# Kernel tuning notes

Measured on AMD Instinct MI355X. Metric: run time of the kernel, lower is better.

## Reference

```python
import jax, jax.numpy as jnp
import numpy as np

NUM_LAYERS = 2
SEQ_LEN = 128
HIDDEN = 512
OUTPUT = 512
BATCH = 512


def setup_inputs() -> dict:
    key = jax.random.key(0)
    ks = jax.random.split(key, 12)
    k = 1.0 / np.sqrt(HIDDEN)
    u = lambda kk, shape: jax.random.uniform(kk, shape, jnp.float32, -k, k)
    return {
        "x": jax.random.normal(ks[0], (BATCH, HIDDEN), jnp.float32),
        # stacked per-layer LSTM params, PyTorch gate order (i, f, g, o)
        "W_ih": u(ks[1], (NUM_LAYERS, 4 * HIDDEN, HIDDEN)),
        "W_hh": u(ks[2], (NUM_LAYERS, 4 * HIDDEN, HIDDEN)),
        "b_ih": u(ks[3], (NUM_LAYERS, 4 * HIDDEN)),
        "b_hh": u(ks[4], (NUM_LAYERS, 4 * HIDDEN)),
        # 3-layer MLP head
        "fc1_w": u(ks[5], (HIDDEN, HIDDEN)),
        "fc1_b": u(ks[6], (HIDDEN,)),
        "fc2_w": u(ks[7], (HIDDEN, HIDDEN)),
        "fc2_b": u(ks[8], (HIDDEN,)),
        "fc3_w": u(ks[9], (OUTPUT, HIDDEN)),
        "fc3_b": u(ks[10], (OUTPUT,)),
    }


def reference(x, W_ih, W_hh, b_ih, b_hh, fc1_w, fc1_b, fc2_w, fc2_b, fc3_w, fc3_b):
    B, H = x.shape
    L = W_ih.shape[0]
    h0 = jnp.zeros((L, B, H), x.dtype)
    c0 = jnp.zeros((L, B, H), x.dtype)

    def step(carry, _):
        h, c, inp = carry  # h,c: [L,B,H]; inp: [B,H]
        x_l = inp
        hs, cs = [], []
        for l in range(L):  # small fixed layer loop
            gates = x_l @ W_ih[l].T + b_ih[l] + h[l] @ W_hh[l].T + b_hh[l]
            i, f, g, o = jnp.split(gates, 4, axis=-1)
            c_new = jax.nn.sigmoid(f) * c[l] + jax.nn.sigmoid(i) * jnp.tanh(g)
            h_new = jax.nn.sigmoid(o) * jnp.tanh(c_new)
            hs.append(h_new)
            cs.append(c_new)
            x_l = h_new
        h = jnp.stack(hs)
        c = jnp.stack(cs)
        h_sum = h.sum(0)  # torch.sum(h_t, 0) over layers
        return (h, c, h_sum), h_sum  # next input is summed hidden

    _, outs = jax.lax.scan(step, (h0, c0, x), None, length=SEQ_LEN)
    out = jnp.transpose(outs, (1, 0, 2))  # [B, seq_len, H]
    out = jax.nn.relu(out @ fc1_w.T + fc1_b)
    out = jax.nn.relu(out @ fc2_w.T + fc2_b)
    out = out @ fc3_w.T + fc3_b  # [B, seq_len, output_size]
    return out
```

## Files before the change

### kernel.cpp

```cpp
#include <hip/hip_runtime.h>
#include <cstdint>
#include <cstddef>


using u16 = unsigned short;
typedef __attribute__((ext_vector_type(8))) _Float16 f16x8;
typedef __attribute__((ext_vector_type(4))) float f32x4;

__device__ __forceinline__ u16 f2h(float f) {
    union { _Float16 h; u16 u; } v; v.h = (_Float16)f; return v.u;
}
__device__ __forceinline__ float h2f(u16 u) {
    union { u16 u; _Float16 h; } v; v.u = u; return (float)v.h;
}
__device__ __forceinline__ float tanh_fast(float v) {
    float a = fabsf(v);
    float t = __expf(-2.f * a);
    float r = (1.f - t) / (1.f + t);
    return copysignf(r, v);
}
__device__ __forceinline__ float sigmoid_fast(float v) {
    return 1.f / (1.f + __expf(-v));
}

__device__ __forceinline__ void gl_lds16(const u16* g, char* l) {
    __builtin_amdgcn_global_load_lds((const __attribute__((address_space(1))) char*)(const char*)g,
                                     (__attribute__((address_space(3))) char*)l, 16, 0, 0);
}

__device__ __forceinline__ f16x8 lds_read_sw(const u16* tile, int row, int cu) {
    int unit = (row << 3) | (cu ^ (row & 7));
    return *(const f16x8*)&tile[unit << 3];
}

__global__ __launch_bounds__(256) void prepack(
    const float* __restrict__ W_ih, const float* __restrict__ W_hh,
    const float* __restrict__ b_ih, const float* __restrict__ b_hh,
    const float* __restrict__ fc1w, const float* __restrict__ fc2w, const float* __restrict__ fc3w,
    u16* __restrict__ Bpack, float* __restrict__ bsumv, u16* __restrict__ fcw)
{
    int stride = gridDim.x * blockDim.x;
    int tid0 = blockIdx.x * blockDim.x + threadIdx.x;
    for (int idx = tid0; idx < 2 * 2048 * 1024; idx += stride) {
        int l = idx >> 21;
        int rem = idx & ((1 << 21) - 1);
        int np = rem >> 10;
        int k = rem & 1023;
        int n = (np & 3) * 512 + (np >> 2);
        float v = (k < 512) ? W_ih[((size_t)l * 2048 + n) * 512 + k]
                            : W_hh[((size_t)l * 2048 + n) * 512 + (k - 512)];
        Bpack[idx] = f2h(v);
    }
    for (int idx = tid0; idx < 2 * 2048; idx += stride) {
        int l = idx >> 11;
        int np = idx & 2047;
        int n = (np & 3) * 512 + (np >> 2);
        bsumv[idx] = b_ih[l * 2048 + n] + b_hh[l * 2048 + n];
    }
    for (int idx = tid0; idx < 3 * 512 * 512; idx += stride) {
        const float* w = idx < 262144 ? fc1w : (idx < 524288 ? fc2w : fc3w);
        fcw[idx] = f2h(w[idx & 262143]);
    }
}

__global__ __launch_bounds__(256) void initbufs(
    const float* __restrict__ x, u16* __restrict__ A0_0, u16* __restrict__ A1_0,
    float* __restrict__ c0, float* __restrict__ c1, float* __restrict__ gb0)
{
    int stride = gridDim.x * blockDim.x;
    int tid0 = blockIdx.x * blockDim.x + threadIdx.x;
    for (int idx = tid0; idx < 512 * 512; idx += stride) {
        int row = idx >> 9, col = idx & 511;
        size_t b = (size_t)row * 1024;
        A0_0[b + col] = f2h(x[idx]);
        A1_0[b + 512 + col] = 0;
        c0[idx] = 0.f;
        c1[idx] = 0.f;
    }
    for (int idx = tid0; idx < 1048576; idx += stride) gb0[idx] = 0.f;
}

template <int IS_L1>
__global__ __launch_bounds__(256) void lstm_phase(
    const u16* __restrict__ Ax, const u16* __restrict__ Ah, int hoffH,
    const u16* __restrict__ Wc, const u16* __restrict__ Wp,
    const float* __restrict__ gbufR, float* __restrict__ gbufW,
    const float* __restrict__ bsumv, float* __restrict__ cbuf,
    u16* __restrict__ hdst, const u16* __restrict__ h0src,
    u16* __restrict__ hsumdst, u16* __restrict__ seqdst)
{
    __shared__ char smem[49152];

    const int id = blockIdx.x;
    const bool isPartial = id >= 256;
    const int rid = id & 255;
    const int xcd = rid & 7, slot = rid >> 3;
    const int nb = xcd * 4 + (slot & 3);
    const int rg = slot >> 2;
    const int n0 = nb * 64;
    const int row0 = rg * 64;
    const int tile = rg * 32 + nb;

    const u16* Abase = isPartial ? Ah : Ax;
    const int xoff = isPartial ? hoffH : 0;
    const u16* Wbase = isPartial ? Wp : Wc;

    const int tid = threadIdx.x;
    const int lane = tid & 63, wid = tid >> 6;
    const int wm = (wid >> 1) * 32, wn = (wid & 1) * 32;
    const int fm = lane & 15, q = lane >> 4;

    const int s0 = wid * 128 + lane, s1 = s0 + 64;
    const int r0s = s0 >> 3, c0s = ((s0 & 7) ^ (r0s & 7)) << 3;
    const int r1s = s1 >> 3, c1s = ((s1 & 7) ^ (r1s & 7)) << 3;
    const size_t aO0 = (size_t)(row0 + r0s) * 1024 + xoff + c0s;
    const size_t aO1 = (size_t)(row0 + r1s) * 1024 + xoff + c1s;
    const size_t bO0 = (size_t)(n0 + r0s) * 1024 + c0s;
    const size_t bO1 = (size_t)(n0 + r1s) * 1024 + c1s;
    const int d0 = wid * 2048, d1 = d0 + 1024;

    f32x4 acc[2][2];
    acc[0][0] = (f32x4)0.f; acc[0][1] = (f32x4)0.f;
    acc[1][0] = (f32x4)0.f; acc[1][1] = (f32x4)0.f;

    auto stage = [&](char* buf, int k0) {
        gl_lds16(Abase + aO0 + k0, buf + d0);
        gl_lds16(Abase + aO1 + k0, buf + d1);
        gl_lds16(Wbase + bO0 + k0, buf + 8192 + d0);
        gl_lds16(Wbase + bO1 + k0, buf + 8192 + d1);
    };

    char* p0 = smem;
    char* p1 = smem + 16384;
    char* p2 = smem + 32768;

    stage(p0, 0);
    stage(p1, 64);

    for (int c = 0; c < 8; ++c) {
        if (c < 7) asm volatile("s_waitcnt vmcnt(4)" ::: "memory");
        else       asm volatile("s_waitcnt vmcnt(0)" ::: "memory");
        __builtin_amdgcn_s_barrier();
        if (c < 6) stage(p2, (c + 2) * 64);
        __builtin_amdgcn_sched_barrier(0);

        const u16* sA = (const u16*)p0;
        const u16* sB = (const u16*)(p0 + 8192);

#pragma unroll
        for (int kf = 0; kf < 2; ++kf) {
            const int cu = kf * 4 + q;
            f16x8 b0 = lds_read_sw(sB, wn + fm, cu);
            f16x8 b1 = lds_read_sw(sB, wn + 16 + fm, cu);
            f16x8 a0 = lds_read_sw(sA, wm + fm, cu);
            f16x8 a1 = lds_read_sw(sA, wm + 16 + fm, cu);
            acc[0][0] = __builtin_amdgcn_mfma_f32_16x16x32_f16(a0, b0, acc[0][0], 0, 0, 0);
            acc[0][1] = __builtin_amdgcn_mfma_f32_16x16x32_f16(a0, b1, acc[0][1], 0, 0, 0);
            acc[1][0] = __builtin_amdgcn_mfma_f32_16x16x32_f16(a1, b0, acc[1][0], 0, 0, 0);
            acc[1][1] = __builtin_amdgcn_mfma_f32_16x16x32_f16(a1, b1, acc[1][1], 0, 0, 0);
        }

        char* t = p0; p0 = p1; p1 = p2; p2 = t;
    }

    if (isPartial) {
        float* dst = gbufW + (size_t)tile * 4096 + wid * 1024 + lane * 4;
        *(f32x4*)(dst +   0) = acc[0][0];
        *(f32x4*)(dst + 256) = acc[0][1];
        *(f32x4*)(dst + 512) = acc[1][0];
        *(f32x4*)(dst + 768) = acc[1][1];
        return;
    }

    {
        const float* src = gbufR + (size_t)tile * 4096 + wid * 1024 + lane * 4;
        acc[0][0] += *(const f32x4*)(src +   0);
        acc[0][1] += *(const f32x4*)(src + 256);
        acc[1][0] += *(const f32x4*)(src + 512);
        acc[1][1] += *(const f32x4*)(src + 768);
    }

    __syncthreads();
    float* sG = (float*)smem;
#pragma unroll
    for (int m = 0; m < 2; ++m)
#pragma unroll
        for (int n = 0; n < 2; ++n)
#pragma unroll
            for (int r = 0; r < 4; ++r) {
                int row = wm + m * 16 + q * 4 + r;
                int col = wn + n * 16 + fm;
                sG[row * 68 + col] = acc[m][n][r];
            }
    __syncthreads();

#pragma unroll
    for (int j = 0; j < 4; ++j) {
        int cell = tid + j * 256;
        int row = cell >> 4, hc = cell & 15;
        const float4 g4 = *(const float4*)&sG[row * 68 + hc * 4];
        const float4 b4 = *(const float4*)&bsumv[n0 + hc * 4];
        float gi = g4.x + b4.x, gf = g4.y + b4.y, gg = g4.z + b4.z, go = g4.w + b4.w;
        int grow = row0 + row;
        int ghc = (n0 >> 2) + hc;
        int cidx = grow * 512 + ghc;
        float c_old = cbuf[cidx];
        float is = sigmoid_fast(gi);
        float fs = sigmoid_fast(gf);
        float os = sigmoid_fast(go);
        float gt = tanh_fast(gg);
        float cn = fs * c_old + is * gt;
        float hn = os * tanh_fast(cn);
        cbuf[cidx] = cn;
        u16 hh = f2h(hn);
        size_t ab = (size_t)grow * 1024;
        if (!IS_L1) {
            hdst[ab + ghc] = hh;
        } else {
            hdst[ab + 512 + ghc] = hh;
            float h0v = h2f(h0src[ab + ghc]);
            float hs = h0v + hn;
            hsumdst[ab + ghc] = f2h(hs);
            seqdst[(size_t)grow * 512 + ghc] = f2h(hs);
        }
    }
}

template <int RELU, int FINAL>
__global__ __launch_bounds__(256) void mlp_gemm(
    const u16* __restrict__ A, const u16* __restrict__ Bw, const float* __restrict__ bias,
    u16* __restrict__ yh, float* __restrict__ yf32)
{
    __shared__ char smem[36864];
    u16* sA = (u16*)smem;
    u16* sB = (u16*)(smem + 9216);

    const int tid = threadIdx.x;
    const int lane = tid & 63, wid = tid >> 6;
    const int row0 = blockIdx.y * 64;
    const int n0 = blockIdx.x * 128;
    const int wn = wid * 32;
    const int fm = lane & 15;
    const int fkbase = (lane >> 4) * 8;

    f32x4 acc[4][2];
#pragma unroll
    for (int m = 0; m < 4; ++m) { acc[m][0] = (f32x4)0.f; acc[m][1] = (f32x4)0.f; }

    for (int kk = 0; kk < 8; ++kk) {
        const int k0 = kk * 64;
        __syncthreads();
#pragma unroll
        for (int r = 0; r < 2; ++r) {
            int c = tid + r * 256;
            int row = c >> 3, cc = (c & 7) * 8;
            *(f16x8*)&sA[row * 72 + cc] = *(const f16x8*)&A[(size_t)(row0 + row) * 512 + k0 + cc];
        }
#pragma unroll
        for (int r = 0; r < 4; ++r) {
            int c = tid + r * 256;
            int row = c >> 3, cc = (c & 7) * 8;
            *(f16x8*)&sB[row * 72 + cc] = *(const f16x8*)&Bw[(size_t)(n0 + row) * 512 + k0 + cc];
        }
        __syncthreads();
#pragma unroll
        for (int kf = 0; kf < 2; ++kf) {
            const int kb = kf * 32 + fkbase;
            f16x8 b0 = *(const f16x8*)&sB[(wn + fm) * 72 + kb];
            f16x8 b1 = *(const f16x8*)&sB[(wn + 16 + fm) * 72 + kb];
#pragma unroll
            for (int m = 0; m < 4; ++m) {
                f16x8 ah = *(const f16x8*)&sA[(m * 16 + fm) * 72 + kb];
                acc[m][0] = __builtin_amdgcn_mfma_f32_16x16x32_f16(ah, b0, acc[m][0], 0, 0, 0);
                acc[m][1] = __builtin_amdgcn_mfma_f32_16x16x32_f16(ah, b1, acc[m][1], 0, 0, 0);
            }
        }
    }

    __syncthreads();
    float* sG = (float*)smem;
#pragma unroll
    for (int m = 0; m < 4; ++m)
#pragma unroll
        for (int n = 0; n < 2; ++n)
#pragma unroll
            for (int r = 0; r < 4; ++r) {
                int row = m * 16 + (lane >> 4) * 4 + r;
                int col = wn + n * 16 + fm;
                sG[row * 132 + col] = acc[m][n][r];
            }
    __syncthreads();

    const int row = tid >> 2;
    const int cg = (tid & 3) * 32;
    const size_t r = (size_t)row0 + row;
#pragma unroll
    for (int c = cg; c < cg + 32; c += 4) {
        float4 g = *(const float4*)&sG[row * 132 + c];
        float4 b = *(const float4*)&bias[n0 + c];
        float v0 = g.x + b.x, v1 = g.y + b.y, v2 = g.z + b.z, v3 = g.w + b.w;
        if (RELU) {
            v0 = fmaxf(v0, 0.f); v1 = fmaxf(v1, 0.f); v2 = fmaxf(v2, 0.f); v3 = fmaxf(v3, 0.f);
        }
        if (!FINAL) {
            ushort4 p;
            p.x = f2h(v0); p.y = f2h(v1); p.z = f2h(v2); p.w = f2h(v3);
            *(ushort4*)&yh[r * 512 + n0 + c] = p;
        } else {
            int tt = (int)(r >> 9), bb = (int)(r & 511);
            float4 o; o.x = v0; o.y = v1; o.z = v2; o.w = v3;
            *(float4*)&yf32[((size_t)bb * 128 + tt) * 512 + n0 + c] = o;
        }
    }
}

extern "C" void kernel_launch(void* const* d_in, const int* in_sizes, int n_in,
                              void* d_out, int out_size, void* d_ws, size_t ws_size,
                              hipStream_t stream) {
    const float* x    = (const float*)d_in[0];
    const float* W_ih = (const float*)d_in[1];
    const float* W_hh = (const float*)d_in[2];
    const float* b_ih = (const float*)d_in[3];
    const float* b_hh = (const float*)d_in[4];
    const float* fc1w = (const float*)d_in[5];
    const float* fc1b = (const float*)d_in[6];
    const float* fc2w = (const float*)d_in[7];
    const float* fc2b = (const float*)d_in[8];
    const float* fc3w = (const float*)d_in[9];
    const float* fc3b = (const float*)d_in[10];

    char* ws = (char*)d_ws;
    u16* Bpack = (u16*)(ws);
    u16* fcw   = (u16*)(ws + 8388608);
    float* bsum = (float*)(ws + 9961472);
    u16* A0[2] = { (u16*)(ws + 9977856),  (u16*)(ws + 11026432) };
    u16* A1[2] = { (u16*)(ws + 12075008), (u16*)(ws + 13123584) };
    float* c0 = (float*)(ws + 14172160);
    float* c1 = (float*)(ws + 15220736);
    u16* seqb = (u16*)(ws + 20463616);
    float* gb[2] = { (float*)(ws + 87572480), (float*)(ws + 87572480 + 4194304) };
    u16* y1   = (u16*)(ws + 87572480);
    float* out = (float*)d_out;

    prepack<<<dim3(512), dim3(256), 0, stream>>>(W_ih, W_hh, b_ih, b_hh, fc1w, fc2w, fc3w,
                                                 Bpack, bsum, fcw);
    initbufs<<<dim3(512), dim3(256), 0, stream>>>(x, A0[0], A1[0], c0, c1, gb[0]);

    const int LSTR = 2048 * 1024;
    for (int s = 0; s < 256; ++s) {
        int t = s >> 1, layer = s & 1, cur = t & 1, nxt = cur ^ 1;
        float* gR = gb[s & 1];
        float* gW = gb[(s + 1) & 1];
        if (!layer) {
            lstm_phase<0><<<dim3(512), dim3(256), 0, stream>>>(
                A0[cur], A1[cur], 512, Bpack, Bpack + LSTR + 512,
                gR, gW, bsum, c0,
                A1[cur], nullptr, nullptr, nullptr);
        } else {
            lstm_phase<1><<<dim3(512), dim3(256), 0, stream>>>(
                A1[cur], A1[cur], 0, Bpack + LSTR, Bpack + 512,
                gR, gW, bsum + 2048, c1,
                A1[nxt], A1[cur], A0[nxt], seqb + (size_t)t * 262144);
        }
    }

    mlp_gemm<1, 0><<<dim3(4, 1024), dim3(256), 0, stream>>>(seqb, fcw, fc1b, y1, nullptr);
    mlp_gemm<1, 0><<<dim3(4, 1024), dim3(256), 0, stream>>>(y1, fcw + 512 * 512, fc2b, seqb, nullptr);
    mlp_gemm<0, 1><<<dim3(4, 1024), dim3(256), 0, stream>>>(seqb, fcw + 2 * 512 * 512, fc3b, nullptr, out);
}
```

Measured before the change: 2.023 ms.

## Load LSTM weight fragments directly to registers and fuse gate epilogue via shuffles

The weight operand is no longer staged through LDS. Each lane now loads its MFMA B fragments straight from global memory into double-buffered registers, which halves the LDS footprint and the per-chunk LDS traffic. The epilogue replaces the shared-memory transpose and its two barriers with lane shuffles that gather the i,f,g,o gates into each lane. s_setprio is wrapped around the MFMA block. The trade-off is that global weight loads are now uncoalesced 16-byte per-lane reads, and the vmcnt counts must match the new outstanding load totals.

```diff
diff --git a/kernel.cpp b/kernel.cpp
--- a/kernel.cpp
+++ b/kernel.cpp
@@ -89,7 +89,7 @@
     u16* __restrict__ hdst, const u16* __restrict__ h0src,
     u16* __restrict__ hsumdst, u16* __restrict__ seqdst)
 {
-    __shared__ char smem[49152];
+    __shared__ char smem[24576];
 
     const int id = blockIdx.x;
     const bool isPartial = id >= 256;
@@ -115,9 +115,10 @@
     const int r1s = s1 >> 3, c1s = ((s1 & 7) ^ (r1s & 7)) << 3;
     const size_t aO0 = (size_t)(row0 + r0s) * 1024 + xoff + c0s;
     const size_t aO1 = (size_t)(row0 + r1s) * 1024 + xoff + c1s;
-    const size_t bO0 = (size_t)(n0 + r0s) * 1024 + c0s;
-    const size_t bO1 = (size_t)(n0 + r1s) * 1024 + c1s;
     const int d0 = wid * 2048, d1 = d0 + 1024;
+
+    const u16* pwA = Wbase + (size_t)(n0 + wn + fm) * 1024 + q * 8;
+    const u16* pwB = pwA + 16 * 1024;
 
     f32x4 acc[2][2];
     acc[0][0] = (f32x4)0.f; acc[0][1] = (f32x4)0.f;
@@ -126,41 +127,53 @@
     auto stage = [&](char* buf, int k0) {
         gl_lds16(Abase + aO0 + k0, buf + d0);
         gl_lds16(Abase + aO1 + k0, buf + d1);
-        gl_lds16(Wbase + bO0 + k0, buf + 8192 + d0);
-        gl_lds16(Wbase + bO1 + k0, buf + 8192 + d1);
     };
 
-    char* p0 = smem;
-    char* p1 = smem + 16384;
-    char* p2 = smem + 32768;
-
-    stage(p0, 0);
-    stage(p1, 64);
-
+    char* bufp[3] = { smem, smem + 8192, smem + 16384 };
+
+    f16x8 w00[2], w01[2], w10[2], w11[2];
+
+    stage(bufp[0], 0);
+    stage(bufp[1], 64);
+    w00[0] = *(const f16x8*)(pwA + 0);
+    w10[0] = *(const f16x8*)(pwA + 32);
+    w01[0] = *(const f16x8*)(pwB + 0);
+    w11[0] = *(const f16x8*)(pwB + 32);
+
+#pragma unroll
     for (int c = 0; c < 8; ++c) {
-        if (c < 7) asm volatile("s_waitcnt vmcnt(4)" ::: "memory");
-        else       asm volatile("s_waitcnt vmcnt(0)" ::: "memory");
+        if (c < 7) asm volatile("s_waitcnt vmcnt(6)" ::: "memory");
+        else       asm volatile("s_waitcnt vmcnt(4)" ::: "memory");
         __builtin_amdgcn_s_barrier();
-        if (c < 6) stage(p2, (c + 2) * 64);
+        if (c + 2 < 8) stage(bufp[(c + 2) % 3], (c + 2) * 64);
+        if (c + 1 < 8) {
+            const int k = (c + 1) * 64;
+            const int p = (c + 1) & 1;
+            w00[p] = *(const f16x8*)(pwA + k);
+            w10[p] = *(const f16x8*)(pwA + k + 32);
+            w01[p] = *(const f16x8*)(pwB + k);
+            w11[p] = *(const f16x8*)(pwB + k + 32);
+        }
         __builtin_amdgcn_sched_barrier(0);
 
-        const u16* sA = (const u16*)p0;
-        const u16* sB = (const u16*)(p0 + 8192);
-
-#pragma unroll
-        for (int kf = 0; kf < 2; ++kf) {
-            const int cu = kf * 4 + q;
-            f16x8 b0 = lds_read_sw(sB, wn + fm, cu);
-            f16x8 b1 = lds_read_sw(sB, wn + 16 + fm, cu);
-            f16x8 a0 = lds_read_sw(sA, wm + fm, cu);
-            f16x8 a1 = lds_read_sw(sA, wm + 16 + fm, cu);
-            acc[0][0] = __builtin_amdgcn_mfma_f32_16x16x32_f16(a0, b0, acc[0][0], 0, 0, 0);
-            acc[0][1] = __builtin_amdgcn_mfma_f32_16x16x32_f16(a0, b1, acc[0][1], 0, 0, 0);
-            acc[1][0] = __builtin_amdgcn_mfma_f32_16x16x32_f16(a1, b0, acc[1][0], 0, 0, 0);
-            acc[1][1] = __builtin_amdgcn_mfma_f32_16x16x32_f16(a1, b1, acc[1][1], 0, 0, 0);
-        }
-
-        char* t = p0; p0 = p1; p1 = p2; p2 = t;
+        const u16* sA = (const u16*)bufp[c % 3];
+        const int p = c & 1;
+
+        f16x8 a00 = lds_read_sw(sA, wm + fm, q);
+        f16x8 a10 = lds_read_sw(sA, wm + 16 + fm, q);
+        f16x8 a01 = lds_read_sw(sA, wm + fm, 4 + q);
+        f16x8 a11 = lds_read_sw(sA, wm + 16 + fm, 4 + q);
+
+        __builtin_amdgcn_s_setprio(1);
+        acc[0][0] = __builtin_amdgcn_mfma_f32_16x16x32_f16(a00, w00[p], acc[0][0], 0, 0, 0);
+        acc[0][1] = __builtin_amdgcn_mfma_f32_16x16x32_f16(a00, w01[p], acc[0][1], 0, 0, 0);
+        acc[1][0] = __builtin_amdgcn_mfma_f32_16x16x32_f16(a10, w00[p], acc[1][0], 0, 0, 0);
+        acc[1][1] = __builtin_amdgcn_mfma_f32_16x16x32_f16(a10, w01[p], acc[1][1], 0, 0, 0);
+        acc[0][0] = __builtin_amdgcn_mfma_f32_16x16x32_f16(a01, w10[p], acc[0][0], 0, 0, 0);
+        acc[0][1] = __builtin_amdgcn_mfma_f32_16x16x32_f16(a01, w11[p], acc[0][1], 0, 0, 0);
+        acc[1][0] = __builtin_amdgcn_mfma_f32_16x16x32_f16(a11, w10[p], acc[1][0], 0, 0, 0);
+        acc[1][1] = __builtin_amdgcn_mfma_f32_16x16x32_f16(a11, w11[p], acc[1][1], 0, 0, 0);
+        __builtin_amdgcn_s_setprio(0);
     }
 
     if (isPartial) {
@@ -180,30 +193,34 @@
         acc[1][1] += *(const f32x4*)(src + 768);
     }
 
-    __syncthreads();
-    float* sG = (float*)smem;
+    const int j = fm & 3;
+    const int hcl = fm >> 2;
 #pragma unroll
     for (int m = 0; m < 2; ++m)
 #pragma unroll
-        for (int n = 0; n < 2; ++n)
-#pragma unroll
-            for (int r = 0; r < 4; ++r) {
-                int row = wm + m * 16 + q * 4 + r;
-                int col = wn + n * 16 + fm;
-                sG[row * 68 + col] = acc[m][n][r];
-            }
-    __syncthreads();
-
-#pragma unroll
-    for (int j = 0; j < 4; ++j) {
-        int cell = tid + j * 256;
-        int row = cell >> 4, hc = cell & 15;
-        const float4 g4 = *(const float4*)&sG[row * 68 + hc * 4];
-        const float4 b4 = *(const float4*)&bsumv[n0 + hc * 4];
-        float gi = g4.x + b4.x, gf = g4.y + b4.y, gg = g4.z + b4.z, go = g4.w + b4.w;
-        int grow = row0 + row;
-        int ghc = (n0 >> 2) + hc;
-        int cidx = grow * 512 + ghc;
+    for (int n = 0; n < 2; ++n) {
+        float v0 = acc[m][n][0], v1 = acc[m][n][1], v2 = acc[m][n][2], v3 = acc[m][n][3];
+        float t0 = __shfl_xor(v1, 1), t1 = __shfl_xor(v0, 1);
+        float t2 = __shfl_xor(v3, 1), t3 = __shfl_xor(v2, 1);
+        bool b1 = (j & 1) != 0;
+        float u0 = b1 ? t0 : v0;
+        float u1 = b1 ? v1 : t1;
+        float u2 = b1 ? t2 : v2;
+        float u3 = b1 ? v3 : t3;
+        t0 = __shfl_xor(u2, 2); t1 = __shfl_xor(u3, 2);
+        t2 = __shfl_xor(u0, 2); t3 = __shfl_xor(u1, 2);
+        bool b2 = (j & 2) != 0;
+        float g0 = b2 ? t0 : u0;
+        float g1 = b2 ? t1 : u1;
+        float g2 = b2 ? u2 : t2;
+        float g3 = b2 ? u3 : t3;
+
+        const int row = row0 + wm + m * 16 + q * 4 + j;
+        const int ghc = ((n0 + wn) >> 2) + n * 4 + hcl;
+        const float4 b4 = *(const float4*)&bsumv[n0 + wn + n * 16 + hcl * 4];
+        float gi = g0 + b4.x, gf = g1 + b4.y, gg = g2 + b4.z, go = g3 + b4.w;
+
+        const int cidx = row * 512 + ghc;
         float c_old = cbuf[cidx];
         float is = sigmoid_fast(gi);
         float fs = sigmoid_fast(gf);
@@ -213,7 +230,7 @@
         float hn = os * tanh_fast(cn);
         cbuf[cidx] = cn;
         u16 hh = f2h(hn);
-        size_t ab = (size_t)grow * 1024;
+        const size_t ab = (size_t)row * 1024;
         if (!IS_L1) {
             hdst[ab + ghc] = hh;
         } else {
@@ -221,7 +238,7 @@
             float h0v = h2f(h0src[ab + ghc]);
             float hs = h0v + hn;
             hsumdst[ab + ghc] = f2h(hs);
-            seqdst[(size_t)grow * 512 + ghc] = f2h(hs);
+            seqdst[(size_t)row * 512 + ghc] = f2h(hs);
         }
     }
 }
```

New measurement: 3.392 ms. +67.7%, slower.

## Double-buffer MLP GEMM tiles with direct global-to-LDS loads and XOR swizzle

Applied to the files above, without the earlier changes.

Rewrites the MLP GEMM main loop so the next K-tile loads directly from global memory into a second LDS buffer while the MFMA work runs on the current one. The padded LDS layout is replaced by an XOR-swizzled layout to avoid bank conflicts. This removes one barrier per iteration and the register round-trip for tile loads. In exchange it doubles the LDS footprint, which may reduce occupancy.

```diff
diff --git a/kernel.cpp b/kernel.cpp
--- a/kernel.cpp
+++ b/kernel.cpp
@@ -231,53 +231,74 @@
     const u16* __restrict__ A, const u16* __restrict__ Bw, const float* __restrict__ bias,
     u16* __restrict__ yh, float* __restrict__ yf32)
 {
-    __shared__ char smem[36864];
-    u16* sA = (u16*)smem;
-    u16* sB = (u16*)(smem + 9216);
+    __shared__ char smem[49152];
 
     const int tid = threadIdx.x;
     const int lane = tid & 63, wid = tid >> 6;
     const int row0 = blockIdx.y * 64;
     const int n0 = blockIdx.x * 128;
     const int wn = wid * 32;
-    const int fm = lane & 15;
-    const int fkbase = (lane >> 4) * 8;
+    const int fm = lane & 15, q = lane >> 4;
+
+    const int sA0 = wid * 128 + lane, sA1 = sA0 + 64;
+    const int rA0 = sA0 >> 3, cA0 = ((sA0 & 7) ^ (rA0 & 7)) << 3;
+    const int rA1 = sA1 >> 3, cA1 = ((sA1 & 7) ^ (rA1 & 7)) << 3;
+    const size_t aO0 = (size_t)(row0 + rA0) * 512 + cA0;
+    const size_t aO1 = (size_t)(row0 + rA1) * 512 + cA1;
+    const int sB0 = wid * 256 + lane;
+    int rB[4], cB[4];
+#pragma unroll
+    for (int i = 0; i < 4; ++i) {
+        int s = sB0 + i * 64;
+        rB[i] = s >> 3; cB[i] = ((s & 7) ^ (rB[i] & 7)) << 3;
+    }
+    const size_t bO0 = (size_t)(n0 + rB[0]) * 512 + cB[0];
+    const size_t bO1 = (size_t)(n0 + rB[1]) * 512 + cB[1];
+    const size_t bO2 = (size_t)(n0 + rB[2]) * 512 + cB[2];
+    const size_t bO3 = (size_t)(n0 + rB[3]) * 512 + cB[3];
+    const int dA0 = wid * 2048, dA1 = dA0 + 1024;
+    const int dB0 = 8192 + wid * 4096;
 
     f32x4 acc[4][2];
 #pragma unroll
     for (int m = 0; m < 4; ++m) { acc[m][0] = (f32x4)0.f; acc[m][1] = (f32x4)0.f; }
 
-    for (int kk = 0; kk < 8; ++kk) {
-        const int k0 = kk * 64;
-        __syncthreads();
-#pragma unroll
-        for (int r = 0; r < 2; ++r) {
-            int c = tid + r * 256;
-            int row = c >> 3, cc = (c & 7) * 8;
-            *(f16x8*)&sA[row * 72 + cc] = *(const f16x8*)&A[(size_t)(row0 + row) * 512 + k0 + cc];
-        }
-#pragma unroll
-        for (int r = 0; r < 4; ++r) {
-            int c = tid + r * 256;
-            int row = c >> 3, cc = (c & 7) * 8;
-            *(f16x8*)&sB[row * 72 + cc] = *(const f16x8*)&Bw[(size_t)(n0 + row) * 512 + k0 + cc];
-        }
-        __syncthreads();
+    auto stage = [&](char* buf, int k0) {
+        gl_lds16(A + aO0 + k0, buf + dA0);
+        gl_lds16(A + aO1 + k0, buf + dA1);
+        gl_lds16(Bw + bO0 + k0, buf + dB0);
+        gl_lds16(Bw + bO1 + k0, buf + dB0 + 1024);
+        gl_lds16(Bw + bO2 + k0, buf + dB0 + 2048);
+        gl_lds16(Bw + bO3 + k0, buf + dB0 + 3072);
+    };
+
+    char* bufs[2] = { smem, smem + 24576 };
+
+    stage(bufs[0], 0);
+    __syncthreads();
+
+    for (int c = 0; c < 8; ++c) {
+        if (c + 1 < 8) stage(bufs[(c + 1) & 1], (c + 1) * 64);
+
+        const u16* sA = (const u16*)bufs[c & 1];
+        const u16* sB = (const u16*)(bufs[c & 1] + 8192);
+
 #pragma unroll
         for (int kf = 0; kf < 2; ++kf) {
-            const int kb = kf * 32 + fkbase;
-            f16x8 b0 = *(const f16x8*)&sB[(wn + fm) * 72 + kb];
-            f16x8 b1 = *(const f16x8*)&sB[(wn + 16 + fm) * 72 + kb];
+            const int cu = kf * 4 + q;
+            f16x8 b0 = lds_read_sw(sB, wn + fm, cu);
+            f16x8 b1 = lds_read_sw(sB, wn + 16 + fm, cu);
 #pragma unroll
             for (int m = 0; m < 4; ++m) {
-                f16x8 ah = *(const f16x8*)&sA[(m * 16 + fm) * 72 + kb];
+                f16x8 ah = lds_read_sw(sA, m * 16 + fm, cu);
                 acc[m][0] = __builtin_amdgcn_mfma_f32_16x16x32_f16(ah, b0, acc[m][0], 0, 0, 0);
                 acc[m][1] = __builtin_amdgcn_mfma_f32_16x16x32_f16(ah, b1, acc[m][1], 0, 0, 0);
             }
         }
-    }
-
-    __syncthreads();
+
+        __syncthreads();
+    }
+
     float* sG = (float*)smem;
 #pragma unroll
     for (int m = 0; m < 4; ++m)
@@ -285,7 +306,7 @@
         for (int n = 0; n < 2; ++n)
 #pragma unroll
             for (int r = 0; r < 4; ++r) {
-                int row = m * 16 + (lane >> 4) * 4 + r;
+                int row = m * 16 + q * 4 + r;
                 int col = wn + n * 16 + fm;
                 sG[row * 132 + col] = acc[m][n][r];
             }
```

New measurement: 2.066 ms. 1.02x slower.

## Swap MFMA operands to keep gates in registers and vectorize h stores

Applied to the files above, without the earlier changes.

The MFMA operands are swapped so that each lane's four accumulator values hold the i, f, g and o gates of one hidden unit. The cell update can then run straight from registers instead of going through an LDS round-trip for the gate tile. The c-state buffer is re-indexed to a hidden-major layout to match the new lane mapping. The new h values are staged in a small LDS tile so the global h, hsum and sequence writes become ushort4 vector stores. A side effect is that the hsum addition now uses the fp16-rounded h rather than the fp32 value.

```diff
diff --git a/kernel.cpp b/kernel.cpp
--- a/kernel.cpp
+++ b/kernel.cpp
@@ -154,10 +154,10 @@
             f16x8 b1 = lds_read_sw(sB, wn + 16 + fm, cu);
             f16x8 a0 = lds_read_sw(sA, wm + fm, cu);
             f16x8 a1 = lds_read_sw(sA, wm + 16 + fm, cu);
-            acc[0][0] = __builtin_amdgcn_mfma_f32_16x16x32_f16(a0, b0, acc[0][0], 0, 0, 0);
-            acc[0][1] = __builtin_amdgcn_mfma_f32_16x16x32_f16(a0, b1, acc[0][1], 0, 0, 0);
-            acc[1][0] = __builtin_amdgcn_mfma_f32_16x16x32_f16(a1, b0, acc[1][0], 0, 0, 0);
-            acc[1][1] = __builtin_amdgcn_mfma_f32_16x16x32_f16(a1, b1, acc[1][1], 0, 0, 0);
+            acc[0][0] = __builtin_amdgcn_mfma_f32_16x16x32_f16(b0, a0, acc[0][0], 0, 0, 0);
+            acc[0][1] = __builtin_amdgcn_mfma_f32_16x16x32_f16(b0, a1, acc[0][1], 0, 0, 0);
+            acc[1][0] = __builtin_amdgcn_mfma_f32_16x16x32_f16(b1, a0, acc[1][0], 0, 0, 0);
+            acc[1][1] = __builtin_amdgcn_mfma_f32_16x16x32_f16(b1, a1, acc[1][1], 0, 0, 0);
         }
 
         char* t = p0; p0 = p1; p1 = p2; p2 = t;
@@ -181,29 +181,20 @@
     }
 
     __syncthreads();
-    float* sG = (float*)smem;
-#pragma unroll
-    for (int m = 0; m < 2; ++m)
-#pragma unroll
-        for (int n = 0; n < 2; ++n)
-#pragma unroll
-            for (int r = 0; r < 4; ++r) {
-                int row = wm + m * 16 + q * 4 + r;
-                int col = wn + n * 16 + fm;
-                sG[row * 68 + col] = acc[m][n][r];
-            }
-    __syncthreads();
-
-#pragma unroll
-    for (int j = 0; j < 4; ++j) {
-        int cell = tid + j * 256;
-        int row = cell >> 4, hc = cell & 15;
-        const float4 g4 = *(const float4*)&sG[row * 68 + hc * 4];
-        const float4 b4 = *(const float4*)&bsumv[n0 + hc * 4];
-        float gi = g4.x + b4.x, gf = g4.y + b4.y, gg = g4.z + b4.z, go = g4.w + b4.w;
-        int grow = row0 + row;
-        int ghc = (n0 >> 2) + hc;
-        int cidx = grow * 512 + ghc;
+    u16* hb = (u16*)smem;
+
+#pragma unroll
+    for (int i = 0; i < 2; ++i)
+#pragma unroll
+    for (int jj = 0; jj < 2; ++jj) {
+        const int hcl = ((wn + i * 16) >> 2) + q;
+        const int bl  = wm + jj * 16 + fm;
+        const float4 b4 = *(const float4*)&bsumv[n0 + wn + i * 16 + q * 4];
+        float gi = acc[i][jj][0] + b4.x;
+        float gf = acc[i][jj][1] + b4.y;
+        float gg = acc[i][jj][2] + b4.z;
+        float go = acc[i][jj][3] + b4.w;
+        const int cidx = ((n0 >> 2) + hcl) * 512 + (row0 + bl);
         float c_old = cbuf[cidx];
         float is = sigmoid_fast(gi);
         float fs = sigmoid_fast(gf);
@@ -212,16 +203,29 @@
         float cn = fs * c_old + is * gt;
         float hn = os * tanh_fast(cn);
         cbuf[cidx] = cn;
-        u16 hh = f2h(hn);
-        size_t ab = (size_t)grow * 1024;
+        hb[bl * 16 + hcl] = f2h(hn);
+    }
+    __syncthreads();
+
+    {
+        const int bl = tid >> 2;
+        const int hc4 = (tid & 3) * 4;
+        const int grow = row0 + bl;
+        const int gh = (n0 >> 2) + hc4;
+        ushort4 h4 = *(const ushort4*)&hb[bl * 16 + hc4];
+        const size_t ab = (size_t)grow * 1024;
         if (!IS_L1) {
-            hdst[ab + ghc] = hh;
+            *(ushort4*)&hdst[ab + gh] = h4;
         } else {
-            hdst[ab + 512 + ghc] = hh;
-            float h0v = h2f(h0src[ab + ghc]);
-            float hs = h0v + hn;
-            hsumdst[ab + ghc] = f2h(hs);
-            seqdst[(size_t)grow * 512 + ghc] = f2h(hs);
+            *(ushort4*)&hdst[ab + 512 + gh] = h4;
+            ushort4 h0v = *(const ushort4*)&h0src[ab + gh];
+            ushort4 s4;
+            s4.x = f2h(h2f(h0v.x) + h2f(h4.x));
+            s4.y = f2h(h2f(h0v.y) + h2f(h4.y));
+            s4.z = f2h(h2f(h0v.z) + h2f(h4.z));
+            s4.w = f2h(h2f(h0v.w) + h2f(h4.w));
+            *(ushort4*)&hsumdst[ab + gh] = s4;
+            *(ushort4*)&seqdst[(size_t)grow * 512 + gh] = s4;
         }
     }
 }
```

After: 1.957 ms. 1.03x faster.
